# Kernel tuning notes

Measured on AMD Instinct MI355X. Metric: run time of the kernel, lower is better.

## Reference

```python
import jax, jax.numpy as jnp
import numpy as np

COST_CLASS = 1.0
COST_MASK = 5.0
COST_DICE = 5.0


def _sample_points(masks, coords):
    """Bilinear grid_sample (align_corners=False, zero padding).

    masks:  [N, H, W] float
    coords: [P, 2] in [0, 1], (x, y) order as in torch grid_sample
    returns [N, P]
    """
    H, W = masks.shape[-2], masks.shape[-1]
    # torch: grid = 2*c - 1; pixel = ((grid+1)*size - 1)/2 = c*size - 0.5
    x = coords[:, 0] * W - 0.5
    y = coords[:, 1] * H - 0.5
    x0 = jnp.floor(x)
    y0 = jnp.floor(y)
    tx = (x - x0).astype(masks.dtype)
    ty = (y - y0).astype(masks.dtype)
    x0i = x0.astype(jnp.int32)
    y0i = y0.astype(jnp.int32)

    def gather(ix, iy):
        valid = ((ix >= 0) & (ix < W) & (iy >= 0) & (iy < H)).astype(masks.dtype)
        v = masks[:, jnp.clip(iy, 0, H - 1), jnp.clip(ix, 0, W - 1)]  # [N, P]
        return v * valid

    v00 = gather(x0i, y0i)
    v01 = gather(x0i + 1, y0i)
    v10 = gather(x0i, y0i + 1)
    v11 = gather(x0i + 1, y0i + 1)
    return (v00 * (1 - tx) * (1 - ty) + v01 * tx * (1 - ty)
            + v10 * (1 - tx) * ty + v11 * tx * ty)


def _cost_one(pred_mask, pred_logits, tgt_mask, labels, coords):
    # pred_mask [Q,H,W], pred_logits [Q,C], tgt_mask [T,H,W], labels [T], coords [P,2]
    probs = jax.nn.softmax(pred_logits, axis=-1)          # [Q, C]
    cost_class = -probs[:, labels]                        # [Q, T]

    pm = _sample_points(pred_mask, coords)                # [Q, P] logits
    tm = _sample_points(tgt_mask, coords)                 # [T, P] in [0,1]
    P = pm.shape[1]

    # pair-wise sigmoid BCE: BCE(x, 1) = softplus(-x), BCE(x, 0) = softplus(x)
    ce_pos = jax.nn.softplus(-pm) / P                     # [Q, P]
    ce_neg = jax.nn.softplus(pm) / P                      # [Q, P]
    cost_mask = ce_pos @ tm.T + ce_neg @ (1.0 - tm).T     # [Q, T]

    # pair-wise dice
    sig = jax.nn.sigmoid(pm)                              # [Q, P]
    numerator = 2.0 * (sig @ tm.T)                        # [Q, T]
    denominator = sig.sum(-1)[:, None] + tm.sum(-1)[None, :]
    cost_dice = 1.0 - (numerator + 1.0) / (denominator + 1.0)

    return COST_MASK * cost_mask + COST_CLASS * cost_class + COST_DICE * cost_dice


def setup_inputs() -> dict:
    key = jax.random.key(0)
    k1, k2, k3, k4, k5 = jax.random.split(key, 5)
    B, Q, C, T, H, W, P = 8, 150, 134, 32, 160, 160, 12544
    masks_queries_logits = jax.random.normal(k1, (B, Q, H, W), dtype=jnp.float32)
    class_queries_logits = jax.random.normal(k2, (B, Q, C), dtype=jnp.float32)
    # binary target masks
    mask_labels = (jax.random.uniform(k3, (B, T, H, W)) > 0.5).astype(jnp.float32)
    class_labels = jax.random.randint(k4, (B, T), 0, 133, dtype=jnp.int64)
    point_coords = jax.random.uniform(k5, (B, P, 2), dtype=jnp.float32)
    return {
        "masks_queries_logits": masks_queries_logits,
        "class_queries_logits": class_queries_logits,
        "mask_labels": mask_labels,
        "class_labels": class_labels,
        "point_coords": point_coords,
    }


def reference(masks_queries_logits, class_queries_logits, mask_labels, class_labels, point_coords):
    # Returns the per-sample cost matrices [B, Q, T] (the GPU-side work of the
    # matcher). The scipy Hungarian assignment on these matrices is CPU-bound
    # and intentionally excluded from the kernel baseline.
    cost = jax.vmap(_cost_one)(
        masks_queries_logits, class_queries_logits, mask_labels, class_labels, point_coords
    )
    return cost
```

## Files before the change

### kernel.cpp

```cpp
#include <hip/hip_runtime.h>
#include <hip/hip_bf16.h>
#include <hip/hip_fp16.h>
#include <math.h>

#define B_ 8
#define Q_ 150
#define QP_ 160
#define C_ 134
#define T_ 32
#define H_ 160
#define W_ 160
#define P_ 12544
#define HW_ (H_ * W_)
#define HW4_ (HW_ / 4)

#define SBLK 1024
#define NPT 12
#define STAIL 256
#define BOFS 51200
#define SEG_ 56
#define KSEG 224
#define KITER 7
#define DSTRIDE (2 * B_ * QP_ * T_)

typedef __attribute__((ext_vector_type(8))) short short8;
typedef __attribute__((ext_vector_type(4))) float floatx4;

__device__ __forceinline__ float waveSum(float v) {
#pragma unroll
  for (int m = 32; m >= 1; m >>= 1) v += __shfl_xor(v, m, 64);
  return v;
}
__device__ __forceinline__ float waveMax(float v) {
#pragma unroll
  for (int m = 32; m >= 1; m >>= 1) v = fmaxf(v, __shfl_xor(v, m, 64));
  return v;
}

__device__ __forceinline__ unsigned short f2bf(float x) {
  union { __hip_bfloat16 h; unsigned short u; } cv;
  cv.h = __float2bfloat16(x);
  return cv.u;
}
__device__ __forceinline__ float bf2f(unsigned short u) {
  return __uint_as_float(((unsigned int)u) << 16);
}
__device__ __forceinline__ float h2f(unsigned u) {
  union { __half h; unsigned short u; } cv;
  cv.u = (unsigned short)u;
  return __half2float(cv.h);
}
__device__ __forceinline__ unsigned short f2h(float x) {
  union { __half h; unsigned short u; } cv;
  cv.h = __float2half(x);
  return cv.u;
}

__launch_bounds__(256) __global__
void samp_kernel(const float* __restrict__ coords,
                 uint4* __restrict__ sPack) {
  int i = blockIdx.x * 256 + threadIdx.x;
  float2 cc = ((const float2*)coords)[i];
  float x = cc.x * (float)W_ - 0.5f;
  float y = cc.y * (float)H_ - 0.5f;
  float x0f = floorf(x), y0f = floorf(y);
  float tx = x - x0f, ty = y - y0f;
  int x0 = (int)x0f, y0 = (int)y0f;

  bool vx0 = (x0 >= 0) && (x0 < W_);
  bool vx1 = (x0 + 1 >= 0) && (x0 + 1 < W_);
  int bx; float wx0, wx1;
  if (vx0) { bx = x0; wx0 = 1.f - tx; wx1 = vx1 ? tx : 0.f; }
  else     { bx = min(max(x0 + 1, 0), W_ - 1); wx0 = vx1 ? tx : 0.f; wx1 = 0.f; }

  bool vy0 = (y0 >= 0) && (y0 < H_);
  bool vy1 = (y0 + 1 >= 0) && (y0 + 1 < H_);
  int by, ir; float wy0, wy1;
  if (vy0) {
    by = y0; wy0 = 1.f - ty;
    if (vy1) { wy1 = ty; ir = 1; } else { wy1 = 0.f; ir = 0; }
  } else {
    by = min(max(y0 + 1, 0), H_ - 1); wy0 = vy1 ? ty : 0.f; wy1 = 0.f; ir = 0;
  }

  int pi = by * W_ + bx;
  unsigned off0 = (unsigned)((pi >> 1) * 4 + (pi & 1) * BOFS);
  uint4 u;
  u.x = off0 | (ir ? (320u << 17) : 0u);
  u.y = (unsigned)f2h(wx0 * wy0) | ((unsigned)f2h(wx1 * wy0) << 16);
  u.z = (unsigned)f2h(wx0 * wy1) | ((unsigned)f2h(wx1 * wy1) << 16);
  u.w = 0u;
  sPack[i] = u;
}

__device__ __forceinline__ float lds2(const unsigned short* img, uint4 pk) {
  unsigned off0 = pk.x & 0x1ffffu;
  unsigned off1 = off0 + (pk.x >> 17);
  unsigned p0 = *(const unsigned*)((const char*)img + off0);
  unsigned p1 = *(const unsigned*)((const char*)img + off1);
  float v00 = __uint_as_float(p0 << 16);
  float v01 = __uint_as_float(p0 & 0xffff0000u);
  float v10 = __uint_as_float(p1 << 16);
  float v11 = __uint_as_float(p1 & 0xffff0000u);
  return h2f(pk.y & 0xffffu) * v00 + h2f(pk.y >> 16) * v01 +
         h2f(pk.z & 0xffffu) * v10 + h2f(pk.z >> 16) * v11;
}

__launch_bounds__(SBLK, 4) __global__
void sample_kernel(const float* __restrict__ masks_q,
                   const float* __restrict__ mask_labels,
                   const uint4* __restrict__ sPack,
                   unsigned short* __restrict__ pmh,
                   unsigned short* __restrict__ tmh,
                   float* __restrict__ S_sp, float* __restrict__ S_sig,
                   float* __restrict__ S_tm) {
  __shared__ unsigned short img[2 * HW_];
  __shared__ float red[32];
  const int x = blockIdx.x;
  const int b = blockIdx.y;
  const int tid = threadIdx.x;
  const bool isPm = (x < Q_);

  const float* src = isPm ? (masks_q + ((size_t)b * Q_ + x) * HW_)
                          : (mask_labels + ((size_t)b * T_ + (x - Q_)) * HW_);
  const float4* s4 = (const float4*)src;
#pragma unroll
  for (int c = 0; c < 6; ++c) {
    int i = c * SBLK + tid;
    float4 v = s4[i];
    float nxt = src[4 * i + 4];
    ushort4 a;
    a.x = f2bf(v.x); a.y = f2bf(v.y); a.z = f2bf(v.z); a.w = f2bf(v.w);
    ushort4 bb;
    bb.x = a.y; bb.y = a.z; bb.z = a.w; bb.w = f2bf(nxt);
    *(ushort4*)&img[4 * i] = a;
    *(ushort4*)&img[HW_ + 4 * i] = bb;
  }
  if (tid < HW4_ - 6 * SBLK) {
    int i = 6 * SBLK + tid;
    float4 v = s4[i];
    float nxt = (i < HW4_ - 1) ? src[4 * i + 4] : 0.f;
    ushort4 a;
    a.x = f2bf(v.x); a.y = f2bf(v.y); a.z = f2bf(v.z); a.w = f2bf(v.w);
    ushort4 bb;
    bb.x = a.y; bb.y = a.z; bb.z = a.w; bb.w = f2bf(nxt);
    *(ushort4*)&img[4 * i] = a;
    *(ushort4*)&img[HW_ + 4 * i] = bb;
  }
  __syncthreads();

  const uint4* sp = sPack + (size_t)b * P_;

  if (isPm) {
    unsigned short* dst = pmh + ((size_t)b * QP_ + x) * P_;
    float ssp = 0.f, ssg = 0.f;
    uint4 pk[NPT];
#pragma unroll
    for (int j = 0; j < NPT; ++j) pk[j] = sp[j * SBLK + tid];
    float v[NPT];
#pragma unroll
    for (int j = 0; j < NPT; ++j) v[j] = lds2(img, pk[j]);
#pragma unroll
    for (int j = 0; j < NPT; ++j) {
      float pm = v[j];
      float e = __expf(-fabsf(pm));
      float r = __builtin_amdgcn_rcpf(1.f + e);
      float sp_ = fmaxf(pm, 0.f) - __logf(r);
      float sg = (pm >= 0.f) ? r : e * r;
      ssp += sp_;
      ssg += sg;
      dst[j * SBLK + tid] = f2bf(pm);
    }
    if (tid < STAIL) {
      int p = NPT * SBLK + tid;
      float pm = lds2(img, sp[p]);
      float e = __expf(-fabsf(pm));
      float r = __builtin_amdgcn_rcpf(1.f + e);
      float sp_ = fmaxf(pm, 0.f) - __logf(r);
      float sg = (pm >= 0.f) ? r : e * r;
      ssp += sp_;
      ssg += sg;
      dst[p] = f2bf(pm);
    }
    ssp = waveSum(ssp);
    ssg = waveSum(ssg);
    int w = tid >> 6;
    if ((tid & 63) == 0) {
      red[w] = ssp;
      red[16 + w] = ssg;
    }
    __syncthreads();
    if (tid == 0) {
      float a = 0.f, bb = 0.f;
#pragma unroll
      for (int i = 0; i < 16; ++i) { a += red[i]; bb += red[16 + i]; }
      S_sp[b * Q_ + x] = a;
      S_sig[b * Q_ + x] = bb;
    }
  } else {
    const int t = x - Q_;
    unsigned short* dst = tmh + ((size_t)b * T_ + t) * P_;
    float stm = 0.f;
    uint4 pk[NPT];
#pragma unroll
    for (int j = 0; j < NPT; ++j) pk[j] = sp[j * SBLK + tid];
    float v[NPT];
#pragma unroll
    for (int j = 0; j < NPT; ++j) v[j] = lds2(img, pk[j]);
#pragma unroll
    for (int j = 0; j < NPT; ++j) {
      stm += v[j];
      dst[j * SBLK + tid] = f2bf(v[j]);
    }
    if (tid < STAIL) {
      int p = NPT * SBLK + tid;
      float vv = lds2(img, sp[p]);
      stm += vv;
      dst[p] = f2bf(vv);
    }
    stm = waveSum(stm);
    int w = tid >> 6;
    if ((tid & 63) == 0) red[w] = stm;
    __syncthreads();
    if (tid == 0) {
      float a = 0.f;
#pragma unroll
      for (int i = 0; i < 16; ++i) a += red[i];
      S_tm[b * T_ + t] = a;
    }
  }
}

__device__ __forceinline__ short8 sig_frag(short8 a) {
  short8 out;
#pragma unroll
  for (int j = 0; j < 8; ++j) {
    float x = bf2f((unsigned short)a[j]);
    float e = __expf(-fabsf(x));
    float r = __builtin_amdgcn_rcpf(1.f + e);
    float sg = (x >= 0.f) ? r : e * r;
    out[j] = (short)f2bf(sg);
  }
  return out;
}

__launch_bounds__(320) __global__
void gemm_kernel(const unsigned short* __restrict__ pmh,
                 const unsigned short* __restrict__ tmh,
                 float* __restrict__ accP) {
  const int b = blockIdx.y;
  const int seg = blockIdx.x;
  const int w = threadIdx.x >> 6;
  const int l = threadIdx.x & 63;
  const int quad = l >> 4;
  const int mrow = l & 15;

  const unsigned short* pmb = pmh + ((size_t)b * QP_ + w * 32) * P_;
  const unsigned short* tmb = tmh + (size_t)b * T_ * P_;

  floatx4 aL[2][2];
  floatx4 aS[2][2];
#pragma unroll
  for (int i = 0; i < 2; ++i)
#pragma unroll
    for (int j = 0; j < 2; ++j) {
      aL[i][j] = (floatx4){0.f, 0.f, 0.f, 0.f};
      aS[i][j] = (floatx4){0.f, 0.f, 0.f, 0.f};
    }

  const int kbase = seg * KSEG;
#pragma unroll
  for (int ki = 0; ki < KITER; ++ki) {
    const int k0 = kbase + ki * 32 + quad * 8;
    short8 a0 = *(const short8*)(pmb + (size_t)(0 * 16 + mrow) * P_ + k0);
    short8 a1 = *(const short8*)(pmb + (size_t)(1 * 16 + mrow) * P_ + k0);
    short8 b0 = *(const short8*)(tmb + (size_t)(0 * 16 + mrow) * P_ + k0);
    short8 b1 = *(const short8*)(tmb + (size_t)(1 * 16 + mrow) * P_ + k0);
    short8 s0 = sig_frag(a0);
    short8 s1 = sig_frag(a1);
    aL[0][0] = __builtin_amdgcn_mfma_f32_16x16x32_bf16(a0, b0, aL[0][0], 0, 0, 0);
    aL[0][1] = __builtin_amdgcn_mfma_f32_16x16x32_bf16(a0, b1, aL[0][1], 0, 0, 0);
    aL[1][0] = __builtin_amdgcn_mfma_f32_16x16x32_bf16(a1, b0, aL[1][0], 0, 0, 0);
    aL[1][1] = __builtin_amdgcn_mfma_f32_16x16x32_bf16(a1, b1, aL[1][1], 0, 0, 0);
    aS[0][0] = __builtin_amdgcn_mfma_f32_16x16x32_bf16(s0, b0, aS[0][0], 0, 0, 0);
    aS[0][1] = __builtin_amdgcn_mfma_f32_16x16x32_bf16(s0, b1, aS[0][1], 0, 0, 0);
    aS[1][0] = __builtin_amdgcn_mfma_f32_16x16x32_bf16(s1, b0, aS[1][0], 0, 0, 0);
    aS[1][1] = __builtin_amdgcn_mfma_f32_16x16x32_bf16(s1, b1, aS[1][1], 0, 0, 0);
  }

  float* base = accP + (size_t)seg * DSTRIDE;
#pragma unroll
  for (int mtl = 0; mtl < 2; ++mtl)
#pragma unroll
    for (int nt = 0; nt < 2; ++nt)
#pragma unroll
      for (int r = 0; r < 4; ++r) {
        int q = w * 32 + mtl * 16 + quad * 4 + r;
        int t = nt * 16 + mrow;
        base[((size_t)(0 * B_ + b) * QP_ + q) * T_ + t] = aL[mtl][nt][r];
        base[((size_t)(1 * B_ + b) * QP_ + q) * T_ + t] = aS[mtl][nt][r];
      }
}

__launch_bounds__(256) __global__
void reduce_kernel(const float* __restrict__ accP, float* __restrict__ accD) {
  int i = blockIdx.x * 256 + threadIdx.x;
  float s = 0.f;
#pragma unroll
  for (int seg = 0; seg < SEG_; ++seg) s += accP[(size_t)seg * DSTRIDE + i];
  accD[i] = s;
}

__launch_bounds__(64) __global__
void final_kernel(const float* __restrict__ class_q,
                  const int* __restrict__ labels,
                  const float* __restrict__ accD,
                  const float* __restrict__ S_sp,
                  const float* __restrict__ S_sig,
                  const float* __restrict__ S_tm,
                  float* __restrict__ out) {
  const int bq = blockIdx.x;
  const int b = bq / Q_;
  const int q = bq % Q_;
  const int l = threadIdx.x;
  const float* cl = class_q + (size_t)bq * C_;

  float v = -INFINITY;
  for (int c = l; c < C_; c += 64) v = fmaxf(v, cl[c]);
  float m = waveMax(v);
  float e = 0.f;
  for (int c = l; c < C_; c += 64) e += __expf(cl[c] - m);
  float den = waveSum(e);

  if (l < T_) {
    int t = l;
    int lbl = labels[b * T_ + t];
    float prob = __expf(cl[lbl] - m) / den;
    float Dlin = accD[((size_t)(0 * B_ + b) * QP_ + q) * T_ + t];
    float Dsig = accD[((size_t)(1 * B_ + b) * QP_ + q) * T_ + t];
    float cmask = (S_sp[bq] - Dlin) * (1.f / (float)P_);
    float dice = 1.f - (2.f * Dsig + 1.f) / (S_sig[bq] + S_tm[b * T_ + t] + 1.f);
    out[(size_t)bq * T_ + t] = 5.f * cmask + 5.f * dice - prob;
  }
}

extern "C" void kernel_launch(void* const* d_in, const int* in_sizes, int n_in,
                              void* d_out, int out_size, void* d_ws,
                              size_t ws_size, hipStream_t stream) {
  const float* masks_q = (const float*)d_in[0];
  const float* class_q = (const float*)d_in[1];
  const float* mask_labels = (const float*)d_in[2];
  const int* class_labels = (const int*)d_in[3];
  const float* coords = (const float*)d_in[4];
  float* out = (float*)d_out;

  float* accD = (float*)d_ws;
  float* accP = accD + DSTRIDE;
  uint4* sPack = (uint4*)(accP + (size_t)SEG_ * DSTRIDE);
  float* S_sp = (float*)(sPack + (size_t)B_ * P_);
  float* S_sig = S_sp + B_ * Q_;
  float* S_tm = S_sig + B_ * Q_;
  unsigned short* pmh = (unsigned short*)(S_tm + B_ * T_);
  unsigned short* tmh = pmh + (size_t)B_ * QP_ * P_;

  samp_kernel<<<(B_ * P_) / 256, 256, 0, stream>>>(coords, sPack);
  sample_kernel<<<dim3(Q_ + T_, B_), SBLK, 0, stream>>>(
      masks_q, mask_labels, sPack, pmh, tmh, S_sp, S_sig, S_tm);
  gemm_kernel<<<dim3(SEG_, B_), 320, 0, stream>>>(pmh, tmh, accP);
  reduce_kernel<<<DSTRIDE / 256, 256, 0, stream>>>(accP, accD);
  final_kernel<<<B_ * Q_, 64, 0, stream>>>(class_q, class_labels, accD, S_sp,
                                           S_sig, S_tm, out);
}
```

Before: 247.2 us.

## Halve sampling LDS image, use four 16-bit gathers, pack paired bf16 stores

Drops the duplicated shifted bf16 image copy in shared memory, so the per-block LDS footprint halves and more blocks can be resident (launch bounds raised to 8). Bilinear sampling now does four 16-bit LDS reads with a per-point x-step flag packed into the offset word, instead of two 32-bit reads from the paired layout. Each thread now handles adjacent point pairs and writes them as one 32-bit store, with a smaller point batch to reduce register pressure. The trade is more LDS load instructions per point in exchange for less staging work and higher occupancy.

```diff
diff --git a/kernel.cpp b/kernel.cpp
--- a/kernel.cpp
+++ b/kernel.cpp
@@ -15,9 +15,8 @@
 #define HW4_ (HW_ / 4)
 
 #define SBLK 1024
-#define NPT 12
-#define STAIL 256
-#define BOFS 51200
+#define NCHUNK 6
+#define TAILP 128
 #define SEG_ 56
 #define KSEG 224
 #define KITER 7
@@ -84,29 +83,30 @@
   }
 
   int pi = by * W_ + bx;
-  unsigned off0 = (unsigned)((pi >> 1) * 4 + (pi & 1) * BOFS);
+  unsigned dxbit = (bx + 1 < W_) ? (1u << 16) : 0u;
+  unsigned dyf = ir ? (320u << 17) : 0u;
   uint4 u;
-  u.x = off0 | (ir ? (320u << 17) : 0u);
+  u.x = (unsigned)(2 * pi) | dxbit | dyf;
   u.y = (unsigned)f2h(wx0 * wy0) | ((unsigned)f2h(wx1 * wy0) << 16);
   u.z = (unsigned)f2h(wx0 * wy1) | ((unsigned)f2h(wx1 * wy1) << 16);
   u.w = 0u;
   sPack[i] = u;
 }
 
-__device__ __forceinline__ float lds2(const unsigned short* img, uint4 pk) {
-  unsigned off0 = pk.x & 0x1ffffu;
-  unsigned off1 = off0 + (pk.x >> 17);
-  unsigned p0 = *(const unsigned*)((const char*)img + off0);
-  unsigned p1 = *(const unsigned*)((const char*)img + off1);
-  float v00 = __uint_as_float(p0 << 16);
-  float v01 = __uint_as_float(p0 & 0xffff0000u);
-  float v10 = __uint_as_float(p1 << 16);
-  float v11 = __uint_as_float(p1 & 0xffff0000u);
-  return h2f(pk.y & 0xffffu) * v00 + h2f(pk.y >> 16) * v01 +
-         h2f(pk.z & 0xffffu) * v10 + h2f(pk.z >> 16) * v11;
-}
-
-__launch_bounds__(SBLK, 4) __global__
+__device__ __forceinline__ float lds4(const unsigned short* img, uint4 pk) {
+  const char* base = (const char*)img;
+  unsigned o00 = pk.x & 0xffffu;
+  unsigned dx2 = (pk.x >> 15) & 2u;
+  unsigned o10 = o00 + (pk.x >> 17);
+  unsigned short v00 = *(const unsigned short*)(base + o00);
+  unsigned short v01 = *(const unsigned short*)(base + o00 + dx2);
+  unsigned short v10 = *(const unsigned short*)(base + o10);
+  unsigned short v11 = *(const unsigned short*)(base + o10 + dx2);
+  return h2f(pk.y & 0xffffu) * bf2f(v00) + h2f(pk.y >> 16) * bf2f(v01) +
+         h2f(pk.z & 0xffffu) * bf2f(v10) + h2f(pk.z >> 16) * bf2f(v11);
+}
+
+__launch_bounds__(SBLK, 8) __global__
 void sample_kernel(const float* __restrict__ masks_q,
                    const float* __restrict__ mask_labels,
                    const uint4* __restrict__ sPack,
@@ -114,7 +114,7 @@
                    unsigned short* __restrict__ tmh,
                    float* __restrict__ S_sp, float* __restrict__ S_sig,
                    float* __restrict__ S_tm) {
-  __shared__ unsigned short img[2 * HW_];
+  __shared__ unsigned short img[HW_];
   __shared__ float red[32];
   const int x = blockIdx.x;
   const int b = blockIdx.y;
@@ -128,24 +128,16 @@
   for (int c = 0; c < 6; ++c) {
     int i = c * SBLK + tid;
     float4 v = s4[i];
-    float nxt = src[4 * i + 4];
-    ushort4 a;
-    a.x = f2bf(v.x); a.y = f2bf(v.y); a.z = f2bf(v.z); a.w = f2bf(v.w);
-    ushort4 bb;
-    bb.x = a.y; bb.y = a.z; bb.z = a.w; bb.w = f2bf(nxt);
-    *(ushort4*)&img[4 * i] = a;
-    *(ushort4*)&img[HW_ + 4 * i] = bb;
+    ushort4 u;
+    u.x = f2bf(v.x); u.y = f2bf(v.y); u.z = f2bf(v.z); u.w = f2bf(v.w);
+    *(ushort4*)&img[4 * i] = u;
   }
   if (tid < HW4_ - 6 * SBLK) {
     int i = 6 * SBLK + tid;
     float4 v = s4[i];
-    float nxt = (i < HW4_ - 1) ? src[4 * i + 4] : 0.f;
-    ushort4 a;
-    a.x = f2bf(v.x); a.y = f2bf(v.y); a.z = f2bf(v.z); a.w = f2bf(v.w);
-    ushort4 bb;
-    bb.x = a.y; bb.y = a.z; bb.z = a.w; bb.w = f2bf(nxt);
-    *(ushort4*)&img[4 * i] = a;
-    *(ushort4*)&img[HW_ + 4 * i] = bb;
+    ushort4 u;
+    u.x = f2bf(v.x); u.y = f2bf(v.y); u.z = f2bf(v.z); u.w = f2bf(v.w);
+    *(ushort4*)&img[4 * i] = u;
   }
   __syncthreads();
 
@@ -153,34 +145,54 @@
 
   if (isPm) {
     unsigned short* dst = pmh + ((size_t)b * QP_ + x) * P_;
+    unsigned* dst32 = (unsigned*)dst;
     float ssp = 0.f, ssg = 0.f;
-    uint4 pk[NPT];
-#pragma unroll
-    for (int j = 0; j < NPT; ++j) pk[j] = sp[j * SBLK + tid];
-    float v[NPT];
-#pragma unroll
-    for (int j = 0; j < NPT; ++j) v[j] = lds2(img, pk[j]);
-#pragma unroll
-    for (int j = 0; j < NPT; ++j) {
-      float pm = v[j];
-      float e = __expf(-fabsf(pm));
-      float r = __builtin_amdgcn_rcpf(1.f + e);
-      float sp_ = fmaxf(pm, 0.f) - __logf(r);
-      float sg = (pm >= 0.f) ? r : e * r;
-      ssp += sp_;
-      ssg += sg;
-      dst[j * SBLK + tid] = f2bf(pm);
-    }
-    if (tid < STAIL) {
-      int p = NPT * SBLK + tid;
-      float pm = lds2(img, sp[p]);
-      float e = __expf(-fabsf(pm));
-      float r = __builtin_amdgcn_rcpf(1.f + e);
-      float sp_ = fmaxf(pm, 0.f) - __logf(r);
-      float sg = (pm >= 0.f) ? r : e * r;
-      ssp += sp_;
-      ssg += sg;
-      dst[p] = f2bf(pm);
+#pragma unroll
+    for (int bat = 0; bat < 2; ++bat) {
+      uint4 pk[6];
+#pragma unroll
+      for (int cc = 0; cc < 3; ++cc) {
+        int p = (bat * 3 + cc) * 2048 + 2 * tid;
+        pk[2 * cc] = sp[p];
+        pk[2 * cc + 1] = sp[p + 1];
+      }
+      float v[6];
+#pragma unroll
+      for (int j = 0; j < 6; ++j) v[j] = lds4(img, pk[j]);
+#pragma unroll
+      for (int cc = 0; cc < 3; ++cc) {
+        unsigned pr = 0;
+#pragma unroll
+        for (int k = 0; k < 2; ++k) {
+          float pm = v[2 * cc + k];
+          float e = __expf(-fabsf(pm));
+          float r = __builtin_amdgcn_rcpf(1.f + e);
+          float sp_ = fmaxf(pm, 0.f) - __logf(r);
+          float sg = (pm >= 0.f) ? r : e * r;
+          ssp += sp_;
+          ssg += sg;
+          pr |= ((unsigned)f2bf(pm)) << (16 * k);
+        }
+        dst32[(bat * 3 + cc) * 1024 + tid] = pr;
+      }
+    }
+    if (tid < TAILP) {
+      int p = NCHUNK * 2048 + 2 * tid;
+      uint4 a = sp[p], c = sp[p + 1];
+      float v0 = lds4(img, a), v1 = lds4(img, c);
+      unsigned pr = 0;
+#pragma unroll
+      for (int k = 0; k < 2; ++k) {
+        float pm = (k == 0) ? v0 : v1;
+        float e = __expf(-fabsf(pm));
+        float r = __builtin_amdgcn_rcpf(1.f + e);
+        float sp_ = fmaxf(pm, 0.f) - __logf(r);
+        float sg = (pm >= 0.f) ? r : e * r;
+        ssp += sp_;
+        ssg += sg;
+        pr |= ((unsigned)f2bf(pm)) << (16 * k);
+      }
+      dst32[(NCHUNK * 2048 + 2 * tid) >> 1] = pr;
     }
     ssp = waveSum(ssp);
     ssg = waveSum(ssg);
@@ -200,23 +212,35 @@
   } else {
     const int t = x - Q_;
     unsigned short* dst = tmh + ((size_t)b * T_ + t) * P_;
+    unsigned* dst32 = (unsigned*)dst;
     float stm = 0.f;
-    uint4 pk[NPT];
-#pragma unroll
-    for (int j = 0; j < NPT; ++j) pk[j] = sp[j * SBLK + tid];
-    float v[NPT];
-#pragma unroll
-    for (int j = 0; j < NPT; ++j) v[j] = lds2(img, pk[j]);
-#pragma unroll
-    for (int j = 0; j < NPT; ++j) {
-      stm += v[j];
-      dst[j * SBLK + tid] = f2bf(v[j]);
-    }
-    if (tid < STAIL) {
-      int p = NPT * SBLK + tid;
-      float vv = lds2(img, sp[p]);
-      stm += vv;
-      dst[p] = f2bf(vv);
+#pragma unroll
+    for (int bat = 0; bat < 2; ++bat) {
+      uint4 pk[6];
+#pragma unroll
+      for (int cc = 0; cc < 3; ++cc) {
+        int p = (bat * 3 + cc) * 2048 + 2 * tid;
+        pk[2 * cc] = sp[p];
+        pk[2 * cc + 1] = sp[p + 1];
+      }
+      float v[6];
+#pragma unroll
+      for (int j = 0; j < 6; ++j) v[j] = lds4(img, pk[j]);
+#pragma unroll
+      for (int cc = 0; cc < 3; ++cc) {
+        float v0 = v[2 * cc], v1 = v[2 * cc + 1];
+        stm += v0 + v1;
+        unsigned pr = (unsigned)f2bf(v0) | (((unsigned)f2bf(v1)) << 16);
+        dst32[(bat * 3 + cc) * 1024 + tid] = pr;
+      }
+    }
+    if (tid < TAILP) {
+      int p = NCHUNK * 2048 + 2 * tid;
+      uint4 a = sp[p], c = sp[p + 1];
+      float v0 = lds4(img, a), v1 = lds4(img, c);
+      stm += v0 + v1;
+      unsigned pr = (unsigned)f2bf(v0) | (((unsigned)f2bf(v1)) << 16);
+      dst32[(NCHUNK * 2048 + 2 * tid) >> 1] = pr;
     }
     stm = waveSum(stm);
     int w = tid >> 6;
```

After: 238.2 us. -3.6%, faster.
